# Kernel optimization log

Hardware: AMD Instinct MI355X
Metric: run time of the kernel (lower is better)

## Reference

```python
import jax, jax.numpy as jnp
import numpy as np

B = 32          # patients
D = 128         # hidden dim (modality_embedding_dim == total_hidden_dim)
H = 4           # attention heads
DH = D // H     # per-head dim
L = 2           # num_graph_layers
N = {'ct': 1024, 'pet': 1024, 'clin': 256, 'gen': 2048, 'pat': 1}
# (src_type, dst_type) for the 8 relation types registered in _setup_relations
REL = [('ct','ct'), ('pet','pet'), ('clin','clin'), ('gen','gen'),
       ('pat','clin'), ('ct','gen'), ('pet','gen'), ('gen','pat')]
E_REL = [8192, 8192, 2048, 16384, 256, 8192, 8192, 2048]
EDGE_NAMES = ['e_ct','e_pet','e_clin','e_gen','e_pat2clin','e_ct2gen','e_pet2gen','e_gen2pat']


def setup_inputs() -> dict:
    key = jax.random.key(0)
    ks = iter(jax.random.split(key, 64))
    nk = lambda: next(ks)
    inp = {}
    inp['x_ct']   = jax.random.normal(nk(), (B, N['ct'],  D), jnp.float32)
    inp['x_pet']  = jax.random.normal(nk(), (B, N['pet'], D), jnp.float32)
    inp['x_clin'] = jax.random.normal(nk(), (B, N['clin'],D), jnp.float32)
    inp['x_gen']  = jax.random.normal(nk(), (B, N['gen'], D), jnp.float32)
    inp['early']  = jax.random.normal(nk(), (B, D), jnp.float32)

    def mk_edges(k, E, ns, nd):
        k1, k2 = jax.random.split(k)
        src = jax.random.randint(k1, (B, 1, E), 0, ns, jnp.int32)
        dst = jax.random.randint(k2, (B, 1, E), 0, nd, jnp.int32)
        return jnp.concatenate([src, dst], axis=1)  # [B,2,E]

    for nm, (s, d), E in zip(EDGE_NAMES, REL, E_REL):
        inp[nm] = mk_edges(nk(), E, N[s], N[d])

    sw = 1.0 / np.sqrt(D)
    inp['W_src'] = jax.random.normal(nk(), (L, 8, D, D), jnp.float32) * sw
    inp['W_dst'] = jax.random.normal(nk(), (L, 8, D, D), jnp.float32) * sw
    inp['a_src'] = jax.random.normal(nk(), (L, 8, H, DH), jnp.float32) * sw
    inp['a_dst'] = jax.random.normal(nk(), (L, 8, H, DH), jnp.float32) * sw
    inp['Wp'] = jax.random.normal(nk(), (3, D, D), jnp.float32) * sw  # CT, PET, genomic pooling
    inp['bp'] = jnp.zeros((3, D), jnp.float32)
    inp['W_sem'] = jax.random.normal(nk(), (4 * D, 128), jnp.float32) * (1.0 / np.sqrt(4 * D))
    inp['b_sem'] = jnp.zeros((128,), jnp.float32)
    inp['q_sem'] = jax.random.normal(nk(), (128,), jnp.float32) * sw
    return inp


def _leaky_relu(x):
    return jnp.where(x > 0, x, 0.2 * x)


def _gat_layer(x, edges, Ws, Wd, As, Ad):
    """One heterogeneous multi-head GAT layer summing over relation types."""
    agg = {t: jnp.zeros((B, N[t], H, DH), jnp.float32) for t in N}
    for r, ((s, d), ei) in enumerate(zip(REL, edges)):
        hs = jnp.einsum('bnd,de->bne', x[s], Ws[r]).reshape(B, N[s], H, DH)
        hd = jnp.einsum('bnd,de->bne', x[d], Wd[r]).reshape(B, N[d], H, DH)
        al_s = jnp.sum(hs * As[r], axis=-1)  # [B,Ns,H]
        al_d = jnp.sum(hd * Ad[r], axis=-1)  # [B,Nd,H]
        nd = N[d]

        def one(hs_b, as_b, ad_b, e_b):
            src, dst = e_b[0], e_b[1]
            logit = _leaky_relu(as_b[src] + ad_b[dst])                      # [E,H]
            m = jnp.full((nd, H), -1e30, logit.dtype).at[dst].max(logit)    # segment max
            p = jnp.exp(logit - m[dst])
            den = jnp.zeros((nd, H), p.dtype).at[dst].add(p)
            w = p / (den[dst] + 1e-16)                                      # edge softmax per dst node
            msg = w[:, :, None] * hs_b[src]                                 # [E,H,DH]
            return jnp.zeros((nd, H, DH), msg.dtype).at[dst].add(msg)

        agg[d] = agg[d] + jax.vmap(one)(hs, al_s, al_d, ei)
    return {t: jax.nn.elu(agg[t].reshape(B, N[t], D)) for t in N}


def _pool(feat, W, b):
    # query = Linear(mean(features)); scores = feat @ q; softmax-weighted sum
    q = jnp.mean(feat, axis=1) @ W + b            # [B,D]
    sc = jnp.einsum('bnd,bd->bn', feat, q)        # [B,N]
    w = jax.nn.softmax(sc, axis=1)
    return jnp.einsum('bn,bnd->bd', w, feat)      # [B,D]


def _forward(x_ct, x_pet, x_clin, x_gen, early, edges,
             W_src, W_dst, a_src, a_dst, Wp, bp, W_sem, b_sem, q_sem):
    x = {'ct': x_ct, 'pet': x_pet, 'clin': x_clin, 'gen': x_gen,
         'pat': early[:, None, :]}
    for l in range(L):
        x = _gat_layer(x, edges, W_src[l], W_dst[l], a_src[l], a_dst[l])
    ct_p  = _pool(x['ct'],  Wp[0], bp[0])
    pet_p = _pool(x['pet'], Wp[1], bp[1])
    gen_p = _pool(x['gen'], Wp[2], bp[2])   # shared across the 3 meta-paths
    pad = jnp.zeros((B, 2 * D), ct_p.dtype)  # pad 2D -> 4D as in original
    imm = jnp.concatenate([ct_p, gen_p, pad], axis=1)
    pro = jnp.concatenate([pet_p, gen_p, pad], axis=1)
    trt = jnp.concatenate([(ct_p + pet_p) * 0.5, gen_p, pad], axis=1)
    z = jnp.stack([imm, pro, trt], axis=1)                     # [B,3,4D]
    s = jnp.einsum('bpa,a->bp', jnp.tanh(jnp.einsum('bpf,fa->bpa', z, W_sem) + b_sem), q_sem)
    beta = jax.nn.softmax(s, axis=1)                           # [B,3]
    fused = jnp.einsum('bp,bpf->bf', beta, z)                  # [B,4D]
    return fused, beta


def reference(x_ct, x_pet, x_clin, x_gen, early,
              e_ct, e_pet, e_clin, e_gen, e_pat2clin, e_ct2gen, e_pet2gen, e_gen2pat,
              W_src, W_dst, a_src, a_dst, Wp, bp, W_sem, b_sem, q_sem):
    edges = [e_ct, e_pet, e_clin, e_gen, e_pat2clin, e_ct2gen, e_pet2gen, e_gen2pat]
    return _forward(x_ct, x_pet, x_clin, x_gen, early, edges,
                    W_src, W_dst, a_src, a_dst, Wp, bp, W_sem, b_sem, q_sem)
```

## Files before the change

kernel.cpp:

```cpp
#include <hip/hip_runtime.h>
#include <math.h>

static constexpr int NB = 32;
static constexpr int ND = 128;

typedef short bf16x8 __attribute__((ext_vector_type(8)));
typedef float f32x4  __attribute__((ext_vector_type(4)));
typedef unsigned short u16x8 __attribute__((ext_vector_type(8)));

__device__ __forceinline__ float lrelu(float x){ return x > 0.f ? x : 0.2f*x; }
__device__ __forceinline__ unsigned short f2b(float f){
  unsigned u = __float_as_uint(f);
  return (unsigned short)((u + 0x7FFFu + ((u>>16)&1u)) >> 16);
}
__device__ __forceinline__ float b2f(unsigned short b){
  return __uint_as_float(((unsigned)b) << 16);
}

__global__ __launch_bounds__(128) void k_fold(const float* __restrict__ Wsrc,
    const float* __restrict__ Wdst, const float* __restrict__ asrc,
    const float* __restrict__ adst, float* __restrict__ vbuf){
  const int wid[5] = {0,1,3,5,6};
  int lr = blockIdx.x, role = blockIdx.y, l = blockIdx.z;
  int r = wid[lr];
  const float* W = (role ? Wdst : Wsrc) + (size_t)(l*8+r)*16384;
  const float* a = (role ? adst : asrc) + (size_t)(l*8+r)*128;
  int k = threadIdx.x;
  float* o = vbuf + ((size_t)((l*5+lr)*2+role))*512 + k*4;
  #pragma unroll
  for(int h=0;h<4;h++){
    float s = 0.f;
    #pragma unroll
    for(int j=0;j<32;j++) s += W[k*128 + h*32 + j]*a[h*32 + j];
    o[h] = s;
  }
}

__global__ __launch_bounds__(256) void k_wpack(const float* __restrict__ Wsrc,
    unsigned short* __restrict__ Wf){
  const int wid[5] = {0,1,3,5,6};
  int lr = blockIdx.x, l = blockIdx.y;
  const float* W = Wsrc + (size_t)(l*8+wid[lr])*16384;
  unsigned short* o = Wf + (size_t)((l*5+lr)*4)*4096;
  for(int idx=threadIdx.x; idx<128*128; idx+=256){
    int k = idx >> 7, col = idx & 127;
    int h = col >> 5, cc = col & 31;
    int k4 = k>>2, g = k4&3, kk = k4>>3, j = 4*((k4>>2)&1) + (k&3);
    int nb = cc>>4, lane = (cc&15) + 16*g;
    o[(size_t)h*4096 + ((size_t)((kk*2+nb)*64 + lane))*8 + j] = f2b(W[k*128 + col]);
  }
}

struct CsrP {
  const int* eg[5];
  int l2E[5];
  int Nd_[5];
  int roff_[5];
  int eoff_[5];
};

__global__ __launch_bounds__(512) void k_csr(CsrP P, int* __restrict__ rowstart,
                                             int* __restrict__ srcidx){
  int b = blockIdx.x, r = blockIdx.y, t = threadIdx.x;
  int E = 1<<P.l2E[r], Nd = P.Nd_[r];
  const int* eg = P.eg[r] + (size_t)b*2*E;
  int* rsO = rowstart + P.roff_[r] + b*(Nd+1);
  int* siO = srcidx + P.eoff_[r] + (size_t)b*E;
  __shared__ int cnt[2048];
  __shared__ int stmp[512];
  for(int i=t;i<Nd;i+=512) cnt[i]=0;
  __syncthreads();
  for(int e=t;e<E;e+=512) atomicAdd(&cnt[eg[E+e]], 1);
  __syncthreads();
  int carry=0;
  for(int c0=0;c0<Nd;c0+=512){
    int idx=c0+t;
    int v=(idx<Nd)?cnt[idx]:0;
    stmp[t]=v; __syncthreads();
    for(int off=1;off<512;off<<=1){
      int u=(t>=off)?stmp[t-off]:0;
      __syncthreads();
      stmp[t]+=u;
      __syncthreads();
    }
    int excl=stmp[t]-v+carry;
    if(idx<Nd){ rsO[idx]=excl; cnt[idx]=excl; }
    int tot = stmp[511];
    __syncthreads();
    carry+=tot;
  }
  if(t==0) rsO[Nd]=carry;
  __syncthreads();
  for(int e=t;e<E;e+=512){
    int src=eg[e], dst=eg[E+e];
    int pos=atomicAdd(&cnt[dst],1);
    siO[pos]=src;
  }
}

struct HsP {
  int tb[4];
  int usef;
  const float* xf[3];
  unsigned long long xoff[3];
  int Ns[3];
  int nW[3];
  unsigned long long wfo[3][2];
  unsigned long long hso[3][2];
  unsigned long long aso[3][2];
  unsigned long long asrco[3][2];
  int nvd[3];
  unsigned long long vdo[3][3];
  unsigned long long aldo2[3][3];
  int ndd[3][3];
};

__global__ __launch_bounds__(256) void k_hs(HsP P, const unsigned short* __restrict__ x16,
    const unsigned short* __restrict__ Wf, const float* __restrict__ asrc,
    const float* __restrict__ vbuf, unsigned short* __restrict__ hs,
    float* __restrict__ als, float* __restrict__ ald){
  __shared__ unsigned short xl[16*132];
  int B = blockIdx.x;
  int t=0; while(t<2 && B>=P.tb[t+1]) t++;
  int local = B - P.tb[t];
  int b = local & 31, tile = local >> 5;
  int n0 = tile*16;
  int tid = threadIdx.x, w = tid>>6, ln = tid&63;
  if(P.usef){
    const float* xf = P.xf[t] + ((size_t)((size_t)b*P.Ns[t] + n0))*128;
    int row = tid>>4, c8 = tid&15;
    float4 a = *(const float4*)(xf + (size_t)row*128 + c8*8);
    float4 c = *(const float4*)(xf + (size_t)row*128 + c8*8 + 4);
    u16x8 r;
    r[0]=f2b(a.x); r[1]=f2b(a.y); r[2]=f2b(a.z); r[3]=f2b(a.w);
    r[4]=f2b(c.x); r[5]=f2b(c.y); r[6]=f2b(c.z); r[7]=f2b(c.w);
    *(u16x8*)&xl[row*132 + c8*8] = r;
  } else {
    int row = tid>>4, ch = tid&15;
    u16x8 v = *(const u16x8*)(x16 + P.xoff[t] + ((size_t)((size_t)b*P.Ns[t] + n0+row)*128 + ch*8));
    *(u16x8*)&xl[row*132 + ch*8] = v;
  }
  __syncthreads();
  int g = ln>>4, r15 = ln&15;
  for(int rep=0; rep<P.nW[t]; rep++){
    const unsigned short* wf = Wf + P.wfo[t][rep] + (size_t)w*4096;
    f32x4 acc[2]; acc[0]=(f32x4){0,0,0,0}; acc[1]=(f32x4){0,0,0,0};
    #pragma unroll
    for(int kk=0;kk<4;kk++){
      const unsigned short* pa = &xl[r15*132 + kk*32 + 4*g];
      ushort4 lo = *(const ushort4*)pa;
      ushort4 hi = *(const ushort4*)(pa+16);
      union { ushort u[8]; bf16x8 v; } tmp;
      tmp.u[0]=lo.x; tmp.u[1]=lo.y; tmp.u[2]=lo.z; tmp.u[3]=lo.w;
      tmp.u[4]=hi.x; tmp.u[5]=hi.y; tmp.u[6]=hi.z; tmp.u[7]=hi.w;
      bf16x8 af = tmp.v;
      #pragma unroll
      for(int nb=0;nb<2;nb++){
        bf16x8 bw = *(const bf16x8*)(wf + ((size_t)((kk*2+nb)*64 + ln))*8);
        acc[nb] = __builtin_amdgcn_mfma_f32_16x16x32_bf16(af, bw, acc[nb], 0, 0, 0);
      }
    }
    unsigned short* ho = hs + P.hso[t][rep] + ((size_t)b*P.Ns[t] + n0)*128;
    #pragma unroll
    for(int qq=0;qq<4;qq++){
      int m = 4*g + qq;
      #pragma unroll
      for(int nb=0;nb<2;nb++){
        ho[(size_t)m*128 + w*32 + nb*16 + r15] = f2b(acc[nb][qq]);
      }
    }
    {
      const float* aS = asrc + P.asrco[t][rep];
      float a0v = aS[w*32 + r15], a1v = aS[w*32 + 16 + r15];
      float p0 = acc[0][0]*a0v + acc[1][0]*a1v;
      float p1 = acc[0][1]*a0v + acc[1][1]*a1v;
      float p2 = acc[0][2]*a0v + acc[1][2]*a1v;
      float p3 = acc[0][3]*a0v + acc[1][3]*a1v;
      #pragma unroll
      for(int off=1; off<16; off<<=1){
        p0 += __shfl_xor(p0,off); p1 += __shfl_xor(p1,off);
        p2 += __shfl_xor(p2,off); p3 += __shfl_xor(p3,off);
      }
      if(r15 < 4){
        float pv = (r15==0)?p0:((r15==1)?p1:((r15==2)?p2:p3));
        als[P.aso[t][rep] + ((size_t)b*P.Ns[t] + n0 + 4*g + r15)*4 + w] = pv;
      }
    }
  }
  int nvd = P.nvd[t];
  if(tid < (nvd<<6)){
    int vd = tid>>6, rem = tid&63, row = rem>>2, h = rem&3;
    const float* vv = vbuf + P.vdo[t][vd];
    float s = 0.f;
    #pragma unroll 8
    for(int k=0;k<128;k++) s += b2f(xl[row*132+k]) * vv[k*4+h];
    ald[P.aldo2[t][vd] + ((size_t)b*P.ndd[t][vd] + n0 + row)*4 + h] = s;
  }
}

static constexpr int MAXE4 = 1536;
static constexpr int WST4  = 1548;

struct Fu5P {
  int nrel[3], ndshift[3];
  int roff[3][3], eoff[3][3], E[3][3], Ns[3][3];
  int rowbase[3][3];
  unsigned long long aldo[3][3];
  unsigned long long outoff[3];
};

__global__ __launch_bounds__(512, 8) void k_fuse5(Fu5P P,
    const int* __restrict__ rowstart, const int* __restrict__ srcidx,
    const float* __restrict__ als, const float* __restrict__ ald,
    const unsigned short* __restrict__ hs, unsigned short* __restrict__ out16){
  __shared__ float wlds[4*WST4];
  __shared__ int   silds[MAXE4];
  __shared__ float aldl[3*256];
  __shared__ int   rsl[3*65];
  __shared__ int   crs[65];
  __shared__ int   cst[3*64];
  int B = blockIdx.x;
  int xcd = B & 7, slot = B >> 3;
  int bg = slot >> 6, rem = slot & 63;
  int b = bg*8 + xcd;
  int t, dtile;
  if(rem < 32){ t = 0; dtile = rem; }
  else if(rem < 48){ t = 1; dtile = rem - 32; }
  else { t = 2; dtile = rem - 48; }
  int Nd = 1 << P.ndshift[t];
  int d0 = dtile * 64;
  int tid = threadIdx.x, w = tid>>6, ln = tid&63;
  int nrel = P.nrel[t];

  for(int q=0;q<nrel;q++){
    const int* rsq = rowstart + P.roff[t][q] + b*(Nd+1) + d0;
    for(int i=tid;i<65;i+=512) rsl[q*65+i] = rsq[i];
    const float* aldq = ald + P.aldo[t][q] + ((size_t)b*Nd + d0)*4;
    for(int i=tid;i<256;i+=512) aldl[(q<<8)+i] = aldq[i];
  }
  __syncthreads();
  if(tid < 65){
    int s = 0;
    for(int q=0;q<nrel;q++) s += rsl[q*65+tid] - rsl[q*65];
    crs[tid] = s;
  } else if(tid >= 128 && tid < 128 + nrel*64){
    int q = (tid-128)>>6, d = (tid-128)&63;
    int s = 0;
    for(int q2=0;q2<nrel;q2++) s += rsl[q2*65+d] - rsl[q2*65];
    for(int q2=0;q2<q;q2++)    s += rsl[q2*65+d+1] - rsl[q2*65+d];
    cst[q*64+d] = s;
  }
  __syncthreads();
  for(int s=tid; s<(nrel<<8); s+=512){
    int q = s>>8, r2 = s&255, dloc = r2>>2, j = r2&3;
    const int* si = srcidx + P.eoff[t][q] + (size_t)b*P.E[t][q];
    int rs0 = rsl[q*65+dloc];
    int deg = rsl[q*65+dloc+1] - rs0;
    int cb = cst[q*64+dloc];
    int bake = P.rowbase[t][q] + b*P.Ns[t][q];
    for(int i=j;i<deg;i+=4) silds[cb+i] = bake + si[rs0+i];
  }
  __syncthreads();
  for(int s=tid; s<(nrel<<8); s+=512){
    int q = s>>8, r2 = s&255, dloc = r2>>2, j = r2&3;
    int deg = rsl[q*65+dloc+1] - rsl[q*65+dloc];
    int cb = cst[q*64+dloc];
    float4 ad4 = *(const float4*)&aldl[(q<<8)+(dloc<<2)];
    for(int i=j;i<deg;i+=4){
      int e = cb+i;
      int sil = silds[e];
      float4 as4 = *(const float4*)(als + 4*(size_t)sil);
      wlds[0*WST4+e] = lrelu(as4.x+ad4.x);
      wlds[1*WST4+e] = lrelu(as4.y+ad4.y);
      wlds[2*WST4+e] = lrelu(as4.z+ad4.z);
      wlds[3*WST4+e] = lrelu(as4.w+ad4.w);
    }
  }
  __syncthreads();
  for(int s=tid; s<(nrel<<8); s+=512){
    int q = s>>8, r2 = s&255, dloc = r2>>2, h2 = r2&3;
    int e0 = cst[q*64+dloc];
    int e1 = e0 + rsl[q*65+dloc+1] - rsl[q*65+dloc];
    float* wrow = &wlds[h2*WST4];
    float m = -1e30f;
    for(int e=e0;e<e1;e++) m = fmaxf(m, wrow[e]);
    float den = 0.f;
    for(int e=e0;e<e1;e++){ float p=__expf(wrow[e]-m); wrow[e]=p; den+=p; }
    float inv = 1.f/(den + 1e-16f);
    for(int e=e0;e<e1;e++) wrow[e] *= inv;
  }
  __syncthreads();
  int h = ln>>4;
  float accA[8], accB[8];
  #pragma unroll
  for(int i=0;i<8;i++){ accA[i]=0.f; accB[i]=0.f; }
  #pragma unroll
  for(int it=0; it<8; it++){
    int dloc = w*8 + it;
    int e0 = crs[dloc], e1 = crs[dloc+1];
    float a0 = 0.f, a1 = 0.f;
    int e = e0;
    int eal = (e0+3)&~3; if(eal > e1) eal = e1;
    for(; e<eal; e++){
      float wv = wlds[h*WST4 + e];
      unsigned v = *(const unsigned*)(hs + ((size_t)silds[e]*128 + 2*ln));
      a0 += wv*__uint_as_float(v<<16);
      a1 += wv*__uint_as_float(v&0xFFFF0000u);
    }
    for(; e+8<=e1; e+=8){
      int4  sq0 = *(const int4*)&silds[e];
      int4  sq1 = *(const int4*)&silds[e+4];
      float4 wq0 = *(const float4*)&wlds[h*WST4 + e];
      float4 wq1 = *(const float4*)&wlds[h*WST4 + e + 4];
      unsigned v0 = *(const unsigned*)(hs + ((size_t)sq0.x*128 + 2*ln));
      unsigned v1 = *(const unsigned*)(hs + ((size_t)sq0.y*128 + 2*ln));
      unsigned v2 = *(const unsigned*)(hs + ((size_t)sq0.z*128 + 2*ln));
      unsigned v3 = *(const unsigned*)(hs + ((size_t)sq0.w*128 + 2*ln));
      unsigned v4 = *(const unsigned*)(hs + ((size_t)sq1.x*128 + 2*ln));
      unsigned v5 = *(const unsigned*)(hs + ((size_t)sq1.y*128 + 2*ln));
      unsigned v6 = *(const unsigned*)(hs + ((size_t)sq1.z*128 + 2*ln));
      unsigned v7 = *(const unsigned*)(hs + ((size_t)sq1.w*128 + 2*ln));
      a0 += wq0.x*__uint_as_float(v0<<16); a1 += wq0.x*__uint_as_float(v0&0xFFFF0000u);
      a0 += wq0.y*__uint_as_float(v1<<16); a1 += wq0.y*__uint_as_float(v1&0xFFFF0000u);
      a0 += wq0.z*__uint_as_float(v2<<16); a1 += wq0.z*__uint_as_float(v2&0xFFFF0000u);
      a0 += wq0.w*__uint_as_float(v3<<16); a1 += wq0.w*__uint_as_float(v3&0xFFFF0000u);
      a0 += wq1.x*__uint_as_float(v4<<16); a1 += wq1.x*__uint_as_float(v4&0xFFFF0000u);
      a0 += wq1.y*__uint_as_float(v5<<16); a1 += wq1.y*__uint_as_float(v5&0xFFFF0000u);
      a0 += wq1.z*__uint_as_float(v6<<16); a1 += wq1.z*__uint_as_float(v6&0xFFFF0000u);
      a0 += wq1.w*__uint_as_float(v7<<16); a1 += wq1.w*__uint_as_float(v7&0xFFFF0000u);
    }
    for(; e+4<=e1; e+=4){
      int4  sq = *(const int4*)&silds[e];
      float4 wq = *(const float4*)&wlds[h*WST4 + e];
      unsigned v0 = *(const unsigned*)(hs + ((size_t)sq.x*128 + 2*ln));
      unsigned v1 = *(const unsigned*)(hs + ((size_t)sq.y*128 + 2*ln));
      unsigned v2 = *(const unsigned*)(hs + ((size_t)sq.z*128 + 2*ln));
      unsigned v3 = *(const unsigned*)(hs + ((size_t)sq.w*128 + 2*ln));
      a0 += wq.x*__uint_as_float(v0<<16); a1 += wq.x*__uint_as_float(v0&0xFFFF0000u);
      a0 += wq.y*__uint_as_float(v1<<16); a1 += wq.y*__uint_as_float(v1&0xFFFF0000u);
      a0 += wq.z*__uint_as_float(v2<<16); a1 += wq.z*__uint_as_float(v2&0xFFFF0000u);
      a0 += wq.w*__uint_as_float(v3<<16); a1 += wq.w*__uint_as_float(v3&0xFFFF0000u);
    }
    for(; e<e1; e++){
      float wv = wlds[h*WST4 + e];
      unsigned v = *(const unsigned*)(hs + ((size_t)silds[e]*128 + 2*ln));
      a0 += wv*__uint_as_float(v<<16);
      a1 += wv*__uint_as_float(v&0xFFFF0000u);
    }
    accA[it] = a0; accB[it] = a1;
  }
  #pragma unroll
  for(int it=0; it<8; it++){
    int m = d0 + w*8 + it;
    float v0 = accA[it], v1 = accB[it];
    v0 = v0 > 0.f ? v0 : expm1f(v0);
    v1 = v1 > 0.f ? v1 : expm1f(v1);
    ushort2 o; o.x = f2b(v0); o.y = f2b(v1);
    *(ushort2*)(out16 + P.outoff[t] + ((size_t)b*Nd + m)*128 + 2*ln) = o;
  }
}

__device__ __constant__ const size_t POFF[3] = {0ull, 4194304ull, 8388608ull};
__device__ __constant__ const int    PNN[3]  = {1024, 1024, 2048};
static constexpr int PCH = 64;
static constexpr int MAXCH = 32;

__global__ __launch_bounds__(128) void k_pool_psum(const unsigned short* __restrict__ x2,
    float* __restrict__ part){
  int p = blockIdx.z, b = blockIdx.x, c = blockIdx.y, t = threadIdx.x;
  int Nn = PNN[p];
  if(c*PCH >= Nn) return;
  const unsigned short* f = x2 + POFF[p] + ((size_t)b*Nn + c*PCH)*ND;
  float acc = 0.f;
  #pragma unroll 8
  for(int n=0;n<PCH;n++) acc += b2f(f[(size_t)n*ND + t]);
  part[(((size_t)p*NB + b)*MAXCH + c)*ND + t] = acc;
}

__global__ __launch_bounds__(128) void k_pool_q(const float* __restrict__ part,
    const float* __restrict__ Wp, const float* __restrict__ bp,
    float* __restrict__ q){
  int p = blockIdx.z, b = blockIdx.x, t = threadIdx.x;
  int nch = PNN[p]/PCH;
  __shared__ float mean[ND];
  float s = 0.f;
  for(int c=0;c<nch;c++) s += part[(((size_t)p*NB + b)*MAXCH + c)*ND + t];
  mean[t] = s / (float)PNN[p];
  __syncthreads();
  const float* W = Wp + (size_t)p*ND*ND;
  float qv = bp[p*ND + t];
  #pragma unroll 8
  for(int k=0;k<ND;k++) qv += mean[k]*W[k*ND + t];
  q[((size_t)p*NB + b)*ND + t] = qv;
}

__global__ __launch_bounds__(256) void k_pool_score(const unsigned short* __restrict__ x2,
    const float* __restrict__ q, float* __restrict__ sc){
  int p = blockIdx.z, b = blockIdx.y;
  int w = threadIdx.x >> 6, lane = threadIdx.x & 63;
  int n = blockIdx.x*4 + w;
  int Nn = PNN[p];
  if(n >= Nn) return;
  const unsigned short* f  = x2 + POFF[p] + ((size_t)b*Nn + n)*ND;
  const float* qb = q + ((size_t)p*NB + b)*ND;
  float s = b2f(f[lane])*qb[lane] + b2f(f[lane+64])*qb[lane+64];
  #pragma unroll
  for(int off=32; off; off>>=1) s += __shfl_xor(s, off);
  if(lane == 0) sc[((size_t)p*NB + b)*2048 + n] = s;
}

__global__ __launch_bounds__(256) void k_pool_smax(const float* __restrict__ sc,
    float* __restrict__ stat){
  int p = blockIdx.z, b = blockIdx.x, t = threadIdx.x;
  int Nn = PNN[p];
  __shared__ float red[256];
  const float* s = sc + ((size_t)p*NB + b)*2048;
  float mx = -1e30f;
  for(int n=t;n<Nn;n+=256) mx = fmaxf(mx, s[n]);
  red[t] = mx; __syncthreads();
  for(int o=128;o;o>>=1){ if(t<o) red[t]=fmaxf(red[t],red[t+o]); __syncthreads(); }
  mx = red[0]; __syncthreads();
  float sum = 0.f;
  for(int n=t;n<Nn;n+=256) sum += __expf(s[n]-mx);
  red[t] = sum; __syncthreads();
  for(int o=128;o;o>>=1){ if(t<o) red[t]+=red[t+o]; __syncthreads(); }
  if(t==0){ stat[((size_t)p*NB + b)*2] = mx; stat[((size_t)p*NB + b)*2+1] = 1.f/red[0]; }
}

__global__ __launch_bounds__(128) void k_pool_wsum(const unsigned short* __restrict__ x2,
    const float* __restrict__ sc, const float* __restrict__ stat,
    float* __restrict__ part){
  int p = blockIdx.z, b = blockIdx.x, c = blockIdx.y, t = threadIdx.x;
  int Nn = PNN[p];
  if(c*PCH >= Nn) return;
  __shared__ float wsh[PCH];
  float mx  = stat[((size_t)p*NB + b)*2];
  float inv = stat[((size_t)p*NB + b)*2+1];
  if(t < PCH) wsh[t] = __expf(sc[((size_t)p*NB + b)*2048 + c*PCH + t] - mx)*inv;
  __syncthreads();
  const unsigned short* f = x2 + POFF[p] + ((size_t)b*Nn + c*PCH)*ND;
  float acc = 0.f;
  #pragma unroll 8
  for(int n=0;n<PCH;n++) acc += wsh[n]*b2f(f[(size_t)n*ND + t]);
  part[(((size_t)p*NB + b)*MAXCH + c)*ND + t] = acc;
}

__global__ __launch_bounds__(128) void k_pool_comb(const float* __restrict__ part,
    float* __restrict__ pooled){
  int p = blockIdx.z, b = blockIdx.x, t = threadIdx.x;
  int nch = PNN[p]/PCH;
  float s = 0.f;
  for(int c=0;c<nch;c++) s += part[(((size_t)p*NB + b)*MAXCH + c)*ND + t];
  pooled[((size_t)p*NB + b)*ND + t] = s;
}

__global__ __launch_bounds__(128) void k_sem(const float* __restrict__ ctp,
    const float* __restrict__ petp, const float* __restrict__ genp,
    const float* __restrict__ Wsem, const float* __restrict__ bsem,
    const float* __restrict__ qsem, float* __restrict__ fused, float* __restrict__ beta){
  int b = blockIdx.x, t = threadIdx.x;
  __shared__ float z[3][256];
  __shared__ float red[128];
  float ct = ctp[b*ND + t], pet = petp[b*ND + t], gen = genp[b*ND + t];
  z[0][t]=ct;  z[1][t]=pet; z[2][t]=0.5f*(ct+pet);
  z[0][ND+t]=gen; z[1][ND+t]=gen; z[2][ND+t]=gen;
  __syncthreads();
  float s[3];
  for(int p=0;p<3;p++){
    float a = bsem[t];
    for(int f=0;f<256;f++) a += z[p][f]*Wsem[f*128 + t];
    a = tanhf(a);
    red[t] = a * qsem[t];
    __syncthreads();
    for(int o=64;o>0;o>>=1){ if(t<o) red[t]+=red[t+o]; __syncthreads(); }
    s[p] = red[0]; __syncthreads();
  }
  float mx = fmaxf(s[0], fmaxf(s[1], s[2]));
  float e0 = __expf(s[0]-mx), e1 = __expf(s[1]-mx), e2 = __expf(s[2]-mx);
  float sm = e0+e1+e2;
  float b0 = e0/sm, b1 = e1/sm, b2 = e2/sm;
  if(t < 3) beta[b*3 + t] = (t==0)?b0:((t==1)?b1:b2);
  float f0 = b0*z[0][t] + b1*z[1][t] + b2*z[2][t];
  float f1 = b0*z[0][ND+t] + b1*z[1][ND+t] + b2*z[2][ND+t];
  fused[(size_t)b*512 + t]       = f0;
  fused[(size_t)b*512 + 128 + t] = f1;
  fused[(size_t)b*512 + 256 + t] = 0.f;
  fused[(size_t)b*512 + 384 + t] = 0.f;
}

extern "C" void kernel_launch(void* const* d_in, const int* in_sizes, int n_in,
                              void* d_out, int out_size, void* d_ws, size_t ws_size,
                              hipStream_t stream) {
  static const int wid[5]    = {0,1,3,5,6};
  static const int edgein[5] = {5,6,8,10,11};
  static const int l2E[5]    = {13,13,14,13,13};
  static const int Nd_l[5]   = {1024,1024,2048,2048,2048};
  static const int E_l[5]    = {8192,8192,16384,8192,8192};
  static const int Ns_l[5]   = {1024,1024,2048,1024,1024};
  static const int eoff[6]   = {0,262144,524288,1048576,1310720,1572864};
  static const int roff[5]   = {0,32800,65600,131168,196736};
  static const unsigned long long aoff[5]   = {0,131072,262144,524288,655360};
  static const unsigned long long aldoff[5] = {0,131072,262144,524288,786432};
  static const unsigned long long hsoff_lr[5] = {0ull,4194304ull,8388608ull,16777216ull,20971520ull};
  static const unsigned long long ALD = 786432;

  const float* Wsrc = (const float*)d_in[13];
  const float* Wp   = (const float*)d_in[17];
  const float* bp   = (const float*)d_in[18];
  const float* Wsem = (const float*)d_in[19];
  const float* bsem = (const float*)d_in[20];
  const float* qsem = (const float*)d_in[21];

  unsigned short* xc16 = (unsigned short*)d_ws;
  unsigned short* x2b16 = xc16;
  unsigned short* xmid16 = xc16 + 16777216;
  float* albase = (float*)(xmid16 + 16777216);
  float* als = albase;
  float* ald = albase + ALD;
  float* vbuf = albase + 1835008;
  unsigned short* wfbuf = (unsigned short*)(vbuf + 10240);
  float* pooled = (float*)(wfbuf + 163840);
  float* part = pooled + 12288;
  float* qbuf = part + 393216;
  float* scbuf = qbuf + 12288;
  float* stat = scbuf + 196608;
  int* rowstart = (int*)(stat + 192);
  int* srcidx = rowstart + 262304;
  unsigned short* hs16 = (unsigned short*)(srcidx + 1572864);

  { dim3 g(5,2,2); k_fold<<<g,128,0,stream>>>(Wsrc, (const float*)d_in[14],
                                              (const float*)d_in[15], (const float*)d_in[16], vbuf); }
  { dim3 g(5,2); k_wpack<<<g,256,0,stream>>>(Wsrc, wfbuf); }

  CsrP csr;
  for(int r=0;r<5;r++){
    csr.eg[r] = (const int*)d_in[edgein[r]];
    csr.l2E[r] = l2E[r]; csr.Nd_[r] = Nd_l[r];
    csr.roff_[r] = roff[r]; csr.eoff_[r] = eoff[r];
  }
  { dim3 g(NB,5); k_csr<<<g,512,0,stream>>>(csr, rowstart, srcidx); }

  static const unsigned long long xoo[3] = {0,4194304,8388608};
  static const int t2_nrel[3] = {3,1,1};
  static const int t2_lrel[3][3] = {{2,3,4},{0,0,0},{1,0,0}};
  static const int t2_nds[3] = {11,10,10};
  static const int t2_out[3] = {2,0,1};

  Fu5P fp;
  for(int t=0;t<3;t++){
    fp.nrel[t]=t2_nrel[t]; fp.ndshift[t]=t2_nds[t]; fp.outoff[t]=xoo[t2_out[t]];
    for(int q=0;q<3;q++){
      int lr = t2_lrel[t][q];
      fp.roff[t][q]=roff[lr]; fp.eoff[t][q]=eoff[lr];
      fp.E[t][q]=E_l[lr]; fp.Ns[t][q]=Ns_l[lr];
      fp.rowbase[t][q]=(int)(aoff[lr]/4);
      fp.aldo[t][q]=aldoff[lr];
    }
  }

  static const int hs_lr[3][2] = {{0,3},{1,4},{2,2}};
  static const int vd_lr[3][3] = {{0,0,0},{1,0,0},{2,3,4}};
  HsP hp;
  hp.tb[0]=0; hp.tb[1]=2048; hp.tb[2]=4096; hp.tb[3]=8192;
  hp.xf[0]=(const float*)d_in[0]; hp.xf[1]=(const float*)d_in[1]; hp.xf[2]=(const float*)d_in[3];
  hp.xoff[0]=0; hp.xoff[1]=4194304; hp.xoff[2]=8388608;
  hp.Ns[0]=1024; hp.Ns[1]=1024; hp.Ns[2]=2048;
  hp.nW[0]=2; hp.nW[1]=2; hp.nW[2]=1;
  hp.nvd[0]=1; hp.nvd[1]=1; hp.nvd[2]=3;
  for(int t=0;t<3;t++){
    for(int rep=0;rep<2;rep++){
      int lr = hs_lr[t][rep];
      hp.hso[t][rep]=hsoff_lr[lr];
      hp.aso[t][rep]=aoff[lr];
    }
    for(int vd=0;vd<3;vd++){
      int lr = vd_lr[t][vd];
      hp.aldo2[t][vd]=aldoff[lr];
      hp.ndd[t][vd]=Nd_l[lr];
    }
  }
  hp.hso[2][1]=0; hp.aso[2][1]=0;

  for(int l=0;l<2;l++){
    unsigned short* xout = (l==0) ? xmid16 : x2b16;
    hp.usef = (l==0) ? 1 : 0;

    for(int t=0;t<3;t++){
      for(int rep=0;rep<2;rep++){
        int lr = hs_lr[t][rep];
        hp.wfo[t][rep]=(unsigned long long)((l*5 + lr)*4)*4096;
        hp.asrco[t][rep]=(unsigned long long)((l*8 + wid[lr])*128);
      }
      for(int vd=0;vd<3;vd++){
        int lr = vd_lr[t][vd];
        hp.vdo[t][vd]=((unsigned long long)((l*5+lr)*2+1))*512;
      }
    }
    k_hs<<<8192,256,0,stream>>>(hp, xmid16, wfbuf, (const float*)d_in[15], vbuf,
                                hs16, als, ald);

    k_fuse5<<<2048,512,0,stream>>>(fp, rowstart, srcidx, als, ald, hs16, xout);
  }

  {
    dim3 gchunk(NB, MAXCH, 3);
    dim3 gone(NB, 1, 3);
    dim3 gscore(512, NB, 3);
    k_pool_psum <<<gchunk,128,0,stream>>>(x2b16, part);
    k_pool_q    <<<gone,  128,0,stream>>>(part, Wp, bp, qbuf);
    k_pool_score<<<gscore,256,0,stream>>>(x2b16, qbuf, scbuf);
    k_pool_smax <<<gone,  256,0,stream>>>(scbuf, stat);
    k_pool_wsum <<<gchunk,128,0,stream>>>(x2b16, scbuf, stat, part);
    k_pool_comb <<<gone,  128,0,stream>>>(part, pooled);
  }

  float* fused = (float*)d_out;
  float* beta  = fused + (size_t)NB*512;
  k_sem<<<NB,128,0,stream>>>(pooled, pooled + NB*ND, pooled + 2*NB*ND,
                             Wsem, bsem, qsem, fused, beta);
}
```

Before: 336.0 us.

## Fuse attention-logit and softmax phases in GAT kernel; use wave-shuffle CSR scan

The aggregation kernel now does source-index baking, leaky-ReLU logits, max, exp and normalisation in one pass per destination row. Each group of four lanes reduces its partial max and sum with xor shuffles, replacing the three block-wide phases and their __syncthreads. Edge offsets are recomputed from rowstart in registers instead of stored in shared arrays, and the ald vector is read straight from global memory. The CSR build replaces a log-step shared-memory scan, which synced every step, with per-thread serial chunks plus a wavefront shuffle scan. The cost is some redundant offset arithmetic and lane imbalance on high-degree rows.

```diff
diff --git a/kernel.cpp b/kernel.cpp
--- a/kernel.cpp
+++ b/kernel.cpp
@@ -67,29 +67,33 @@
   int* rsO = rowstart + P.roff_[r] + b*(Nd+1);
   int* siO = srcidx + P.eoff_[r] + (size_t)b*E;
   __shared__ int cnt[2048];
-  __shared__ int stmp[512];
+  __shared__ int wsums[8];
   for(int i=t;i<Nd;i+=512) cnt[i]=0;
   __syncthreads();
   for(int e=t;e<E;e+=512) atomicAdd(&cnt[eg[E+e]], 1);
   __syncthreads();
-  int carry=0;
-  for(int c0=0;c0<Nd;c0+=512){
-    int idx=c0+t;
-    int v=(idx<Nd)?cnt[idx]:0;
-    stmp[t]=v; __syncthreads();
-    for(int off=1;off<512;off<<=1){
-      int u=(t>=off)?stmp[t-off]:0;
-      __syncthreads();
-      stmp[t]+=u;
-      __syncthreads();
-    }
-    int excl=stmp[t]-v+carry;
-    if(idx<Nd){ rsO[idx]=excl; cnt[idx]=excl; }
-    int tot = stmp[511];
-    __syncthreads();
-    carry+=tot;
-  }
-  if(t==0) rsO[Nd]=carry;
+  int C = Nd >> 9;
+  int base = t*C;
+  int loc[4]; int s_=0;
+  for(int i=0;i<C;i++){ loc[i]=cnt[base+i]; s_+=loc[i]; }
+  int lane = t&63, wv = t>>6;
+  int sinc = s_;
+  #pragma unroll
+  for(int off=1;off<64;off<<=1){
+    int u = __shfl_up(sinc, off);
+    if(lane>=off) sinc += u;
+  }
+  if(lane==63) wsums[wv]=sinc;
+  __syncthreads();
+  int wbase=0, total=0;
+  #pragma unroll
+  for(int i=0;i<8;i++){ int v=wsums[i]; if(i<wv) wbase+=v; total+=v; }
+  int excl = wbase + sinc - s_;
+  for(int i=0;i<C;i++){
+    int idx=base+i;
+    rsO[idx]=excl; cnt[idx]=excl; excl+=loc[i];
+  }
+  if(t==0) rsO[Nd]=total;
   __syncthreads();
   for(int e=t;e<E;e+=512){
     int src=eg[e], dst=eg[E+e];
@@ -209,16 +213,13 @@
   unsigned long long outoff[3];
 };
 
-__global__ __launch_bounds__(512, 8) void k_fuse5(Fu5P P,
+__global__ __launch_bounds__(512, 8) void k_fuse6(Fu5P P,
     const int* __restrict__ rowstart, const int* __restrict__ srcidx,
     const float* __restrict__ als, const float* __restrict__ ald,
     const unsigned short* __restrict__ hs, unsigned short* __restrict__ out16){
   __shared__ float wlds[4*WST4];
   __shared__ int   silds[MAXE4];
-  __shared__ float aldl[3*256];
   __shared__ int   rsl[3*65];
-  __shared__ int   crs[65];
-  __shared__ int   cst[3*64];
   int B = blockIdx.x;
   int xcd = B & 7, slot = B >> 3;
   int bg = slot >> 6, rem = slot & 63;
@@ -235,61 +236,57 @@
   for(int q=0;q<nrel;q++){
     const int* rsq = rowstart + P.roff[t][q] + b*(Nd+1) + d0;
     for(int i=tid;i<65;i+=512) rsl[q*65+i] = rsq[i];
-    const float* aldq = ald + P.aldo[t][q] + ((size_t)b*Nd + d0)*4;
-    for(int i=tid;i<256;i+=512) aldl[(q<<8)+i] = aldq[i];
-  }
-  __syncthreads();
-  if(tid < 65){
-    int s = 0;
-    for(int q=0;q<nrel;q++) s += rsl[q*65+tid] - rsl[q*65];
-    crs[tid] = s;
-  } else if(tid >= 128 && tid < 128 + nrel*64){
-    int q = (tid-128)>>6, d = (tid-128)&63;
-    int s = 0;
-    for(int q2=0;q2<nrel;q2++) s += rsl[q2*65+d] - rsl[q2*65];
-    for(int q2=0;q2<q;q2++)    s += rsl[q2*65+d+1] - rsl[q2*65+d];
-    cst[q*64+d] = s;
-  }
-  __syncthreads();
+  }
+  __syncthreads();
+
   for(int s=tid; s<(nrel<<8); s+=512){
     int q = s>>8, r2 = s&255, dloc = r2>>2, j = r2&3;
-    const int* si = srcidx + P.eoff[t][q] + (size_t)b*P.E[t][q];
     int rs0 = rsl[q*65+dloc];
     int deg = rsl[q*65+dloc+1] - rs0;
-    int cb = cst[q*64+dloc];
+    int cb = 0;
+    for(int q2=0;q2<nrel;q2++) cb += rsl[q2*65+dloc] - rsl[q2*65];
+    for(int q2=0;q2<q;q2++)    cb += rsl[q2*65+dloc+1] - rsl[q2*65+dloc];
+    const int* si = srcidx + P.eoff[t][q] + (size_t)b*P.E[t][q];
     int bake = P.rowbase[t][q] + b*P.Ns[t][q];
-    for(int i=j;i<deg;i+=4) silds[cb+i] = bake + si[rs0+i];
-  }
-  __syncthreads();
-  for(int s=tid; s<(nrel<<8); s+=512){
-    int q = s>>8, r2 = s&255, dloc = r2>>2, j = r2&3;
-    int deg = rsl[q*65+dloc+1] - rsl[q*65+dloc];
-    int cb = cst[q*64+dloc];
-    float4 ad4 = *(const float4*)&aldl[(q<<8)+(dloc<<2)];
+    float4 ad4 = *(const float4*)(ald + P.aldo[t][q] + ((size_t)b*Nd + d0 + dloc)*4);
+    float m0=-1e30f,m1=-1e30f,m2=-1e30f,m3=-1e30f;
     for(int i=j;i<deg;i+=4){
       int e = cb+i;
-      int sil = silds[e];
+      int sil = bake + si[rs0+i];
+      silds[e] = sil;
       float4 as4 = *(const float4*)(als + 4*(size_t)sil);
-      wlds[0*WST4+e] = lrelu(as4.x+ad4.x);
-      wlds[1*WST4+e] = lrelu(as4.y+ad4.y);
-      wlds[2*WST4+e] = lrelu(as4.z+ad4.z);
-      wlds[3*WST4+e] = lrelu(as4.w+ad4.w);
-    }
-  }
-  __syncthreads();
-  for(int s=tid; s<(nrel<<8); s+=512){
-    int q = s>>8, r2 = s&255, dloc = r2>>2, h2 = r2&3;
-    int e0 = cst[q*64+dloc];
-    int e1 = e0 + rsl[q*65+dloc+1] - rsl[q*65+dloc];
-    float* wrow = &wlds[h2*WST4];
-    float m = -1e30f;
-    for(int e=e0;e<e1;e++) m = fmaxf(m, wrow[e]);
-    float den = 0.f;
-    for(int e=e0;e<e1;e++){ float p=__expf(wrow[e]-m); wrow[e]=p; den+=p; }
-    float inv = 1.f/(den + 1e-16f);
-    for(int e=e0;e<e1;e++) wrow[e] *= inv;
-  }
-  __syncthreads();
+      float l0=lrelu(as4.x+ad4.x), l1=lrelu(as4.y+ad4.y);
+      float l2=lrelu(as4.z+ad4.z), l3=lrelu(as4.w+ad4.w);
+      wlds[0*WST4+e]=l0; wlds[1*WST4+e]=l1;
+      wlds[2*WST4+e]=l2; wlds[3*WST4+e]=l3;
+      m0=fmaxf(m0,l0); m1=fmaxf(m1,l1); m2=fmaxf(m2,l2); m3=fmaxf(m3,l3);
+    }
+    m0=fmaxf(m0,__shfl_xor(m0,1)); m1=fmaxf(m1,__shfl_xor(m1,1));
+    m2=fmaxf(m2,__shfl_xor(m2,1)); m3=fmaxf(m3,__shfl_xor(m3,1));
+    m0=fmaxf(m0,__shfl_xor(m0,2)); m1=fmaxf(m1,__shfl_xor(m1,2));
+    m2=fmaxf(m2,__shfl_xor(m2,2)); m3=fmaxf(m3,__shfl_xor(m3,2));
+    float n0_=0.f,n1_=0.f,n2_=0.f,n3_=0.f;
+    for(int i=j;i<deg;i+=4){
+      int e = cb+i;
+      float p0=__expf(wlds[0*WST4+e]-m0); wlds[0*WST4+e]=p0; n0_+=p0;
+      float p1=__expf(wlds[1*WST4+e]-m1); wlds[1*WST4+e]=p1; n1_+=p1;
+      float p2=__expf(wlds[2*WST4+e]-m2); wlds[2*WST4+e]=p2; n2_+=p2;
+      float p3=__expf(wlds[3*WST4+e]-m3); wlds[3*WST4+e]=p3; n3_+=p3;
+    }
+    n0_+=__shfl_xor(n0_,1); n1_+=__shfl_xor(n1_,1);
+    n2_+=__shfl_xor(n2_,1); n3_+=__shfl_xor(n3_,1);
+    n0_+=__shfl_xor(n0_,2); n1_+=__shfl_xor(n1_,2);
+    n2_+=__shfl_xor(n2_,2); n3_+=__shfl_xor(n3_,2);
+    float i0=1.f/(n0_+1e-16f), i1=1.f/(n1_+1e-16f);
+    float i2=1.f/(n2_+1e-16f), i3=1.f/(n3_+1e-16f);
+    for(int i=j;i<deg;i+=4){
+      int e = cb+i;
+      wlds[0*WST4+e]*=i0; wlds[1*WST4+e]*=i1;
+      wlds[2*WST4+e]*=i2; wlds[3*WST4+e]*=i3;
+    }
+  }
+  __syncthreads();
+
   int h = ln>>4;
   float accA[8], accB[8];
   #pragma unroll
@@ -297,7 +294,12 @@
   #pragma unroll
   for(int it=0; it<8; it++){
     int dloc = w*8 + it;
-    int e0 = crs[dloc], e1 = crs[dloc+1];
+    int e0=0, e1=0;
+    for(int q2=0;q2<nrel;q2++){
+      int r0 = rsl[q2*65];
+      e0 += rsl[q2*65+dloc]   - r0;
+      e1 += rsl[q2*65+dloc+1] - r0;
+    }
     float a0 = 0.f, a1 = 0.f;
     int e = e0;
     int eal = (e0+3)&~3; if(eal > e1) eal = e1;
@@ -599,7 +601,7 @@
     k_hs<<<8192,256,0,stream>>>(hp, xmid16, wfbuf, (const float*)d_in[15], vbuf,
                                 hs16, als, ald);
 
-    k_fuse5<<<2048,512,0,stream>>>(fp, rowstart, srcidx, als, ald, hs16, xout);
+    k_fuse6<<<2048,512,0,stream>>>(fp, rowstart, srcidx, als, ald, hs16, xout);
   }
 
   {
```

Result: no change. 331.7 us (-1.3%).
